# Performance work log

Measured on AMD Instinct MI355X. Metric: run time of the kernel, lower is better.

Reference implementation:

```python
import jax, jax.numpy as jnp
import numpy as np

EMBED_DIM = 512
NUM_HEADS = 8
B, L_Q, L_K = 2, 2048, 2048


def setup_inputs() -> dict:
    key = jax.random.key(0)
    ks = jax.random.split(key, 8)
    s = 0.02  # weight init scale
    return {
        "query": jax.random.normal(ks[0], (B, L_Q, EMBED_DIM), jnp.float32),
        "key":   jax.random.normal(ks[1], (B, L_K, EMBED_DIM), jnp.float32),
        "value": jax.random.normal(ks[2], (B, L_K, EMBED_DIM), jnp.float32),
        "wq": jax.random.normal(ks[3], (EMBED_DIM, EMBED_DIM), jnp.float32) * s,
        "wk": jax.random.normal(ks[4], (EMBED_DIM, EMBED_DIM), jnp.float32) * s,
        "wv": jax.random.normal(ks[5], (EMBED_DIM, EMBED_DIM), jnp.float32) * s,
        "bq": jnp.zeros((EMBED_DIM,), jnp.float32),
        "bk": jnp.zeros((EMBED_DIM,), jnp.float32),
        "bv": jnp.zeros((EMBED_DIM,), jnp.float32),
        "wo": jax.random.normal(ks[6], (EMBED_DIM, EMBED_DIM), jnp.float32) * s,
        "bo": jnp.zeros((EMBED_DIM,), jnp.float32),
    }


def _prob_sparse_mask(query, key, num_heads):
    # Faithful to _prob_QK: max-mean sparsity score, top-k query selection,
    # gather of reduced queries, reduced QK matmul (vectorized, no python loops).
    Bq, Lq, D = query.shape
    Lk = key.shape[1]
    dh = D // num_heads
    n_top = int(np.log(Lk))  # int(np.ceil/np.log) as in source forward: int(np.log(L_K))
    Q = query.reshape(Bq, Lq, num_heads, dh)
    K = key.reshape(Bq, Lk, num_heads, dh)
    Qh = jnp.transpose(Q, (0, 2, 1, 3))                      # [B,H,Lq,dh]
    # NOTE: source does K.transpose(1,2).reshape(B,H,D,L_K) -- a reshape, not a
    # transpose of the last two dims. We replicate that exactly.
    Kr = jnp.transpose(K, (0, 2, 1, 3)).reshape(Bq, num_heads, dh, Lk)  # [B,H,dh,Lk]
    QK = jnp.einsum('bhqd,bhdk->bhqk', Qh, Kr)               # [B,H,Lq,Lk]
    M = QK.max(-1) - QK.sum(-1) / Lk                         # max-mean score [B,H,Lq]
    _, M_top = jax.lax.top_k(M, n_top)                       # [B,H,n_top]
    Q_red = jnp.take_along_axis(Qh, M_top[..., None], axis=2)  # [B,H,n_top,dh]
    QK_red = jnp.einsum('bhtd,bhdk->bhtk', Q_red, Kr)        # [B,H,n_top,Lk]
    # Scatter reduced rows back into a full additive attn mask (zeros elsewhere).
    mask = jnp.zeros((Bq, num_heads, Lq, Lk), QK.dtype)
    bi = jnp.arange(Bq)[:, None, None]
    hi = jnp.arange(num_heads)[None, :, None]
    return mask.at[bi, hi, M_top].set(QK_red)


def reference(query, key, value, wq, wk, wv, bq, bk, bv, wo, bo):
    Bq, Lq, D = query.shape
    Lk = key.shape[1]
    H = NUM_HEADS
    dh = D // H
    mask = _prob_sparse_mask(query, key, H)                  # [B,H,Lq,Lk]
    q = (query @ wq.T + bq).reshape(Bq, Lq, H, dh).transpose(0, 2, 1, 3)
    k = (key @ wk.T + bk).reshape(Bq, Lk, H, dh).transpose(0, 2, 1, 3)
    v = (value @ wv.T + bv).reshape(Bq, Lk, H, dh).transpose(0, 2, 1, 3)
    scores = jnp.einsum('bhqd,bhkd->bhqk', q, k) * (dh ** -0.5) + mask
    attn = jax.nn.softmax(scores, axis=-1)                   # dropout inactive (eval)
    out = jnp.einsum('bhqk,bhkd->bhqd', attn, v)
    out = out.transpose(0, 2, 1, 3).reshape(Bq, Lq, D)
    return out @ wo.T + bo
```

## Files before the change

kernel.cpp:

```cpp
#include <hip/hip_runtime.h>
#include <type_traits>

#define DEV static __device__ __forceinline__

typedef short s16;
typedef __attribute__((ext_vector_type(4))) short short4_t;
typedef __attribute__((ext_vector_type(8))) short short8;
typedef __attribute__((ext_vector_type(4))) float f32x4;
typedef __attribute__((ext_vector_type(16))) float f32x16;

#define NB 2
#define NH 8
#define SL 2048
#define DM 512
#define DH 64
#define NTOP 7
#define LOG2E 1.4426950408889634f
#define NROWS (NB*NH*SL)
#define FSPLIT 4
#define SSPLIT 4

DEV short f2bf(float x){
  union { float f; unsigned u; } v; v.f = x;
  unsigned r = v.u + 0x7fffu + ((v.u >> 16) & 1u);
  return (short)(r >> 16);
}
DEV float bf2f(short b){
  union { float f; unsigned u; } v; v.u = ((unsigned)(unsigned short)b) << 16;
  return v.f;
}
DEV f32x4 mfma16(short8 a, short8 b, f32x4 c){
  return __builtin_amdgcn_mfma_f32_16x16x32_bf16(a, b, c, 0, 0, 0);
}
DEV f32x16 mfma32(short8 a, short8 b, f32x16 c){
  return __builtin_amdgcn_mfma_f32_32x32x16_bf16(a, b, c, 0, 0, 0);
}
DEV unsigned cvtpk(float lo, float hi){
  unsigned r;
  asm("v_cvt_pk_bf16_f32 %0, %1, %2" : "=v"(r) : "v"(lo), "v"(hi));
  return r;
}
DEV void gl2lds16(const s16* g, s16* l){
  __builtin_amdgcn_global_load_lds(
      (const __attribute__((address_space(1))) unsigned*)g,
      (__attribute__((address_space(3))) unsigned*)l, 16, 0, 0);
}

__global__ void prep_kernel(const float* __restrict__ query, const float* __restrict__ key,
    const float* __restrict__ value,
    const float* __restrict__ wq, const float* __restrict__ wk,
    const float* __restrict__ wv, const float* __restrict__ wo,
    s16* __restrict__ q_hi, s16* __restrict__ q_lo, s16* __restrict__ xk, s16* __restrict__ xv,
    s16* __restrict__ khi, s16* __restrict__ klo,
    s16* __restrict__ wqb, s16* __restrict__ wkb, s16* __restrict__ wvb, s16* __restrict__ wob){
  const int nbb = (NB*SL*DM)/256;
  const int wbb = (DM*DM)/256;
  __shared__ s16 thi[64][66];
  __shared__ s16 tlo[64][66];
  int bid = blockIdx.x;
  int t = threadIdx.x;
  if (bid < nbb){
    int i = bid*256 + t;
    float v = query[i];
    short h = f2bf(v);
    q_hi[i] = h;
    q_lo[i] = f2bf(v - bf2f(h));
    return;
  }
  bid -= nbb;
  if (bid < nbb){ int i = bid*256 + t; xk[i] = f2bf(key[i]); return; }
  bid -= nbb;
  if (bid < nbb){ int i = bid*256 + t; xv[i] = f2bf(value[i]); return; }
  bid -= nbb;
  if (bid < 512){
    int k6 = bid & 31, h = (bid >> 5) & 7, b = bid >> 8;
    int kl = t & 63, dq = t >> 6;
    #pragma unroll
    for (int dd = 0; dd < 16; ++dd){
      int d = dd*4 + dq;
      float v = key[((size_t)b*SL + d*32 + k6)*DM + h*DH + kl];
      short hh = f2bf(v);
      thi[d][kl] = hh;
      tlo[d][kl] = f2bf(v - bf2f(hh));
    }
    __syncthreads();
    int d2 = t & 63, kq = t >> 6;
    size_t obase = (((size_t)(b*NH + h))*SL + (size_t)k6*64)*DH;
    #pragma unroll
    for (int kk = 0; kk < 16; ++kk){
      int kl2 = kk*4 + kq;
      khi[obase + (size_t)kl2*DH + d2] = thi[d2][kl2];
      klo[obase + (size_t)kl2*DH + d2] = tlo[d2][kl2];
    }
    return;
  }
  bid -= 512;
  if (bid < wbb){ int i = bid*256 + t; wqb[i] = f2bf(wq[i]); return; }
  bid -= wbb;
  if (bid < wbb){ int i = bid*256 + t; wkb[i] = f2bf(wk[i]); return; }
  bid -= wbb;
  if (bid < wbb){ int i = bid*256 + t; wvb[i] = f2bf(wv[i]); return; }
  bid -= wbb;
  if (bid < wbb){ int i = bid*256 + t; wob[i] = f2bf(wo[i]); return; }
}

__global__ __launch_bounds__(256) void vpt_kernel(const s16* __restrict__ Vp, s16* __restrict__ VpT){
  __shared__ s16 tl[64][66];
  int bid = blockIdx.x;
  int k6 = bid & 31, h = (bid >> 5) & 7, b = bid >> 8;
  int t = threadIdx.x;
  int d = t & 63, kq = t >> 6;
  #pragma unroll
  for (int kk = 0; kk < 16; ++kk){
    int kl = kk*4 + kq;
    tl[kl][d] = Vp[((size_t)b*SL + k6*64 + kl)*DM + h*DH + d];
  }
  __syncthreads();
  int kl2 = t & 63, dq = t >> 6;
  size_t obase = ((size_t)(b*NH + h))*DH*SL + (size_t)k6*64;
  #pragma unroll
  for (int dd = 0; dd < 16; ++dd){
    int d2 = dd*4 + dq;
    VpT[obase + (size_t)d2*SL + kl2] = tl[kl2][d2];
  }
}

template<int OUTF32>
DEV void gemm_body(const s16* __restrict__ A, const s16* __restrict__ Bw,
        const float* __restrict__ bias, void* __restrict__ Cout, int bid, int tid, float scale){
  __shared__ __align__(16) s16 Abuf[2][128*64];
  __shared__ __align__(16) s16 Bbuf[2][64*64];
  int nt = bid >> 3, ot = bid & 7;
  int w = tid >> 6, l = tid & 63;
  int lr = l & 15, lg = l >> 4;
  int n0 = nt*128, o0 = ot*64;
  auto stage = [&](int cur, int kg){
    #pragma unroll
    for (int i = 0; i < 4; ++i){
      int r = w*32 + i*8 + (l>>3);
      int cs = (l&7) ^ (r&7);
      gl2lds16(A + (size_t)(n0 + r)*DM + kg + cs*8, &Abuf[cur][(w*32 + i*8)*64]);
    }
    #pragma unroll
    for (int i = 0; i < 2; ++i){
      int r = w*16 + i*8 + (l>>3);
      int cs = (l&7) ^ (r&7);
      gl2lds16(Bw + (size_t)(o0 + r)*DM + kg + cs*8, &Bbuf[cur][(w*16 + i*8)*64]);
    }
  };
  f32x4 acc[2][4] = {};
  stage(0, 0);
  __syncthreads();
  const int NIT = DM/64;
  for (int it = 0; it < NIT; ++it){
    int cur = it & 1;
    if (it + 1 < NIT) stage(cur^1, (it+1)*64);
    #pragma unroll
    for (int kc = 0; kc < 2; ++kc){
      short8 a0 = *(const short8*)&Abuf[cur][(w*32 +      lr)*64 + ((kc*4+lg) ^ (lr&7))*8];
      short8 a1 = *(const short8*)&Abuf[cur][(w*32 + 16 + lr)*64 + ((kc*4+lg) ^ (lr&7))*8];
      #pragma unroll
      for (int c = 0; c < 4; ++c){
        short8 bf = *(const short8*)&Bbuf[cur][(c*16 + lr)*64 + ((kc*4+lg) ^ (lr&7))*8];
        acc[0][c] = mfma16(a0, bf, acc[0][c]);
        acc[1][c] = mfma16(a1, bf, acc[1][c]);
      }
    }
    __syncthreads();
  }
  #pragma unroll
  for (int sub = 0; sub < 2; ++sub)
    #pragma unroll
    for (int c = 0; c < 4; ++c){
      int col = o0 + c*16 + lr;
      float bb = bias[col];
      #pragma unroll
      for (int j = 0; j < 4; ++j){
        int row = n0 + w*32 + sub*16 + lg*4 + j;
        float v = (acc[sub][c][j] + bb)*scale;
        if (OUTF32) ((float*)Cout)[(size_t)row*DM + col] = v;
        else        ((s16*) Cout)[(size_t)row*DM + col] = f2bf(v);
      }
    }
}

__global__ __launch_bounds__(256) void gemm_proj(const s16* __restrict__ Aq, const s16* __restrict__ Ak,
        const s16* __restrict__ Av, const s16* __restrict__ Wq, const s16* __restrict__ Wk,
        const s16* __restrict__ Wv, const float* __restrict__ bq, const float* __restrict__ bk,
        const float* __restrict__ bv, s16* __restrict__ Oq, s16* __restrict__ Ok, s16* __restrict__ Ov){
  int which = blockIdx.x >> 8;
  const s16* A  = which == 0 ? Aq : which == 1 ? Ak : Av;
  const s16* Bw = which == 0 ? Wq : which == 1 ? Wk : Wv;
  const float* bias = which == 0 ? bq : which == 1 ? bk : bv;
  s16* C = which == 0 ? Oq : which == 1 ? Ok : Ov;
  float scale = which == 0 ? 0.125f*LOG2E : 1.0f;
  gemm_body<0>(A, Bw, bias, C, blockIdx.x & 255, threadIdx.x, scale);
}

__global__ __launch_bounds__(256) void gemm_out(const s16* __restrict__ A, const s16* __restrict__ Bw,
        const float* __restrict__ bias, float* __restrict__ Cout){
  gemm_body<1>(A, Bw, bias, Cout, blockIdx.x, threadIdx.x, 1.0f);
}

__global__ __launch_bounds__(512) void stats_kernel(const s16* __restrict__ qhi, const s16* __restrict__ qlo,
        const s16* __restrict__ khi, const s16* __restrict__ klo,
        float* __restrict__ Mmx, float* __restrict__ Msm){
  __shared__ __align__(16) s16 Hbuf[2][64*64];
  __shared__ __align__(16) s16 Lbuf[2][64*64];
  int bid = blockIdx.x;
  int s = bid & 3, qt = (bid >> 2) & 15, h = (bid >> 6) & 7, b = bid >> 9;
  int tid = threadIdx.x;
  int w = tid >> 6, l = tid & 63;
  int lr = l & 15, lg = l >> 4;
  int dx = lr & 7;
  int q0 = qt*128 + w*16;
  const s16* qp  = qhi + ((size_t)b*SL + q0 + lr)*DM + h*DH + lg*8;
  const s16* qlp = qlo + ((size_t)b*SL + q0 + lr)*DM + h*DH + lg*8;
  short8 qh0 = *(const short8*)qp;
  short8 qh1 = *(const short8*)(qp + 32);
  short8 ql0 = *(const short8*)qlp;
  short8 ql1 = *(const short8*)(qlp + 32);
  const s16* kb  = khi + ((size_t)b*NH + h)*SL*DH;
  const s16* klb = klo + ((size_t)b*NH + h)*SL*DH;
  const s16* hR0 = &Hbuf[0][lr*64 + ((lg      ^ dx)*8)];
  const s16* hR1 = &Hbuf[0][lr*64 + (((4+lg) ^ dx)*8)];
  const s16* lR0 = &Lbuf[0][lr*64 + ((lg      ^ dx)*8)];
  const s16* lR1 = &Lbuf[0][lr*64 + (((4+lg) ^ dx)*8)];
  int rS = tid >> 3;
  int slot = tid & 7;
  int cs = slot ^ (rS & 7);
  int kbeg = s*(SL/SSPLIT);
  const int NT = (SL/SSPLIT)/64;
  f32x4 hreg, lreg;
  auto loadr = [&](int t){
    int kg = kbeg + t*64;
    hreg = *(const f32x4*)(kb  + (size_t)(kg + rS)*DH + cs*8);
    lreg = *(const f32x4*)(klb + (size_t)(kg + rS)*DH + cs*8);
  };
  auto writer = [&](int buf){
    *(f32x4*)&Hbuf[buf][rS*64 + slot*8] = hreg;
    *(f32x4*)&Lbuf[buf][rS*64 + slot*8] = lreg;
  };
  float mx = -1e30f, sm = 0.f;
  auto body = [&](auto CURC){
    constexpr int CUR = decltype(CURC)::value;
    #pragma unroll
    for (int t = 0; t < 4; ++t){
      short8 kh0 = *(const short8*)(hR0 + CUR*4096 + t*1024);
      short8 kh1 = *(const short8*)(hR1 + CUR*4096 + t*1024);
      short8 kl0 = *(const short8*)(lR0 + CUR*4096 + t*1024);
      short8 kl1 = *(const short8*)(lR1 + CUR*4096 + t*1024);
      f32x4 sacc = {};
      sacc = mfma16(kh0, qh0, sacc);
      sacc = mfma16(kh1, qh1, sacc);
      sacc = mfma16(kl0, qh0, sacc);
      sacc = mfma16(kl1, qh1, sacc);
      sacc = mfma16(kh0, ql0, sacc);
      sacc = mfma16(kh1, ql1, sacc);
      #pragma unroll
      for (int j = 0; j < 4; ++j){ mx = fmaxf(mx, sacc[j]); sm += sacc[j]; }
    }
  };
  loadr(0);
  writer(0);
  loadr(1);
  __syncthreads();
  auto step = [&](auto TC){
    constexpr int T = decltype(TC)::value;
    if constexpr (T + 1 < NT) writer((T+1)&1);
    if constexpr (T + 2 < NT) loadr(T+2);
    body(std::integral_constant<int, T&1>{});
    __syncthreads();
  };
  step(std::integral_constant<int,0>{}); step(std::integral_constant<int,1>{});
  step(std::integral_constant<int,2>{}); step(std::integral_constant<int,3>{});
  step(std::integral_constant<int,4>{}); step(std::integral_constant<int,5>{});
  step(std::integral_constant<int,6>{}); step(std::integral_constant<int,7>{});
  mx = fmaxf(mx, __shfl_xor(mx, 16));
  mx = fmaxf(mx, __shfl_xor(mx, 32));
  sm += __shfl_xor(sm, 16);
  sm += __shfl_xor(sm, 32);
  if (lg == 0){
    size_t row = ((size_t)b*NH + h)*SL + q0 + lr;
    Mmx[(size_t)s*NROWS + row] = mx;
    Msm[(size_t)s*NROWS + row] = sm;
  }
}

__global__ __launch_bounds__(256) void topk_kernel(const float* __restrict__ Mmx,
        const float* __restrict__ Msm, int* __restrict__ topidx, int* __restrict__ rowsel){
  int bh = blockIdx.x;
  int t = threadIdx.x;
  int w = t >> 6, l = t & 63;
  __shared__ float smv[SL];
  __shared__ float rv[4];
  __shared__ int   ri[4];
  size_t base = (size_t)bh*SL;
  for (int i = t; i < SL; i += 256){
    float mx = Mmx[base + i];
    float sm = Msm[base + i];
    #pragma unroll
    for (int s = 1; s < SSPLIT; ++s){
      mx = fmaxf(mx, Mmx[(size_t)s*NROWS + base + i]);
      sm += Msm[(size_t)s*NROWS + base + i];
    }
    smv[i] = mx - sm*(1.0f/SL);
    rowsel[base + i] = -1;
  }
  __syncthreads();
  for (int tt = 0; tt < NTOP; ++tt){
    float bvv = -1e38f; int bi = SL;
    for (int i = t; i < SL; i += 256){
      float v = smv[i];
      if (v > bvv){ bvv = v; bi = i; }
    }
    #pragma unroll
    for (int off = 32; off >= 1; off >>= 1){
      float ov = __shfl_xor(bvv, off);
      int oi = __shfl_xor(bi, off);
      if (ov > bvv || (ov == bvv && oi < bi)){ bvv = ov; bi = oi; }
    }
    if (l == 0){ rv[w] = bvv; ri[w] = bi; }
    __syncthreads();
    if (t == 0){
      float bv2 = rv[0]; int bi2 = ri[0];
      #pragma unroll
      for (int ww = 1; ww < 4; ++ww)
        if (rv[ww] > bv2 || (rv[ww] == bv2 && ri[ww] < bi2)){ bv2 = rv[ww]; bi2 = ri[ww]; }
      topidx[bh*8 + tt] = bi2;
      rowsel[base + bi2] = tt;
      smv[bi2] = -1e38f;
    }
    __syncthreads();
  }
}

__global__ __launch_bounds__(256) void maskrow_kernel(const float* __restrict__ query,
        const float* __restrict__ key, const int* __restrict__ topidx, float* __restrict__ maskrows){
  __shared__ float tile[64][65];
  __shared__ float qs[NTOP][64];
  int bid = blockIdx.x;
  int k6 = bid & 31, h = (bid >> 5) & 7, b = bid >> 8;
  int bh = b*NH + h;
  int t = threadIdx.x;
  int kl = t & 63, w = t >> 6;
  for (int i = t; i < NTOP*64; i += 256){
    int tt = i >> 6, d = i & 63;
    qs[tt][d] = query[((size_t)b*SL + topidx[bh*8 + tt])*DM + h*DH + d];
  }
  #pragma unroll
  for (int dd = 0; dd < 16; ++dd){
    int d = dd*4 + w;
    tile[d][kl] = key[((size_t)b*SL + d*32 + k6)*DM + h*DH + kl];
  }
  __syncthreads();
  for (int tt = w; tt < NTOP; tt += 4){
    float acc = 0.f;
    #pragma unroll
    for (int d = 0; d < 64; ++d)
      acc = fmaf(qs[tt][d], tile[d][kl], acc);
    maskrows[((size_t)bh*NTOP + tt)*SL + k6*64 + kl] = acc*LOG2E;
  }
}

__global__ __launch_bounds__(256, 3) void flash_kernel(const s16* __restrict__ Qp,
        const s16* __restrict__ Kp, const s16* __restrict__ VpT,
        const float* __restrict__ maskrows, const int* __restrict__ rowsel,
        float* __restrict__ Opart, float* __restrict__ lpart){
  __shared__ __align__(16) s16 SB[4*64*64];
  int bid = blockIdx.x;
  int s = bid & 3, qt = (bid >> 2) & 15, h = (bid >> 6) & 7, b = bid >> 9;
  int tid = threadIdx.x;
  int w = tid >> 6, l = tid & 63;
  int ln = l & 31, lh = l >> 5;
  int q0 = qt*128 + w*32;
  int bh = b*NH + h;
  const s16* qp = Qp + ((size_t)b*SL + q0 + ln)*DM + h*DH + lh*8;
  short8 bq[4];
  #pragma unroll
  for (int kc = 0; kc < 4; ++kc) bq[kc] = *(const short8*)(qp + kc*16);
  int sel = rowsel[(size_t)bh*SL + q0 + ln];
  const float* mrow = maskrows + ((size_t)bh*NTOP + (sel >= 0 ? sel : 0))*SL;
  const s16* kpb = Kp + (size_t)b*SL*DM + h*DH;
  const s16* vtb = VpT + (size_t)bh*DH*SL;
  const s16* kR[2][4];
  #pragma unroll
  for (int g = 0; g < 2; ++g)
    #pragma unroll
    for (int kc = 0; kc < 4; ++kc)
      kR[g][kc] = &SB[(g*32 + ln)*64 + (((kc*2 + lh) ^ (ln & 7))*8)];
  int r8 = l >> 3;
  int slot = l & 7;
  int cs = slot ^ (r8 & 7);
  int kbeg = s*(SL/FSPLIT);
  const int NT = (SL/FSPLIT)/64;
  f32x4 kreg[2], vreg[2];
  auto loadr = [&](int t){
    int kg = kbeg + t*64;
    #pragma unroll
    for (int c = 0; c < 2; ++c){
      int r = c*32 + w*8 + r8;
      kreg[c] = *(const f32x4*)(kpb + (size_t)(kg + r)*DM + cs*8);
      vreg[c] = *(const f32x4*)(vtb + (size_t)r*SL + kg + cs*8);
    }
  };
  auto writer = [&](int buf){
    #pragma unroll
    for (int c = 0; c < 2; ++c){
      int r = c*32 + w*8 + r8;
      *(f32x4*)&SB[(size_t)buf*4096 + r*64 + slot*8] = kreg[c];
      *(f32x4*)&SB[8192 + (size_t)buf*4096 + r*64 + slot*8] = vreg[c];
    }
  };
  short8 ones;
  #pragma unroll
  for (int i = 0; i < 8; ++i) ones[i] = (short)0x3F80;
  f32x16 accO[2] = {};
  f32x16 accL = {};
  auto body = [&](auto CURC, int k0){
    constexpr int CB = decltype(CURC)::value * 8192;
    f32x16 S[2] = {};
    __builtin_amdgcn_s_setprio(1);
    #pragma unroll
    for (int g = 0; g < 2; ++g)
      #pragma unroll
      for (int kc = 0; kc < 4; ++kc){
        short8 kf = *(const short8*)((const char*)kR[g][kc] + CB);
        S[g] = mfma32(kf, bq[kc], S[g]);
      }
    __builtin_amdgcn_s_setprio(0);
    if (sel >= 0){
      #pragma unroll
      for (int g = 0; g < 2; ++g)
        #pragma unroll
        for (int rq = 0; rq < 4; ++rq)
          #pragma unroll
          for (int j = 0; j < 4; ++j)
            S[g][rq*4 + j] += mrow[k0 + g*32 + rq*8 + lh*4 + j];
    }
    #pragma unroll
    for (int g = 0; g < 2; ++g)
      #pragma unroll
      for (int e = 0; e < 16; ++e)
        S[g][e] = exp2f(S[g][e]);
    unsigned W[2][8];
    #pragma unroll
    for (int g = 0; g < 2; ++g)
      #pragma unroll
      for (int t = 0; t < 8; ++t)
        W[g][t] = cvtpk(S[g][2*t], S[g][2*t+1]);
    short8 pf[4];
    #pragma unroll
    for (int kc = 0; kc < 4; ++kc){
      int g = kc >> 1, j = kc & 1;
      unsigned a0 = W[g][4*j + 0], a1 = W[g][4*j + 2];
      asm("v_permlane32_swap_b32 %0, %1" : "+v"(a0), "+v"(a1));
      unsigned b0 = W[g][4*j + 1], b1 = W[g][4*j + 3];
      asm("v_permlane32_swap_b32 %0, %1" : "+v"(b0), "+v"(b1));
      union { unsigned u[4]; short8 s8; } uu;
      uu.u[0] = a0; uu.u[1] = b0; uu.u[2] = a1; uu.u[3] = b1;
      pf[kc] = uu.s8;
    }
    __builtin_amdgcn_s_setprio(1);
    #pragma unroll
    for (int kc = 0; kc < 4; ++kc)
      accL = mfma32(ones, pf[kc], accL);
    #pragma unroll
    for (int dg = 0; dg < 2; ++dg)
      #pragma unroll
      for (int kc = 0; kc < 4; ++kc){
        short8 vf = *(const short8*)((const char*)kR[dg][kc] + CB + 16384);
        accO[dg] = mfma32(vf, pf[kc], accO[dg]);
      }
    __builtin_amdgcn_s_setprio(0);
  };
  loadr(0);
  writer(0);
  loadr(1);
  __syncthreads();
  auto step = [&](auto TC){
    constexpr int T = decltype(TC)::value;
    if constexpr (T + 1 < NT) writer((T+1)&1);
    if constexpr (T + 2 < NT) loadr(T+2);
    body(std::integral_constant<int, T&1>{}, kbeg + T*64);
    __syncthreads();
  };
  step(std::integral_constant<int,0>{}); step(std::integral_constant<int,1>{});
  step(std::integral_constant<int,2>{}); step(std::integral_constant<int,3>{});
  step(std::integral_constant<int,4>{}); step(std::integral_constant<int,5>{});
  step(std::integral_constant<int,6>{}); step(std::integral_constant<int,7>{});
  size_t row = (size_t)bh*SL + q0 + ln;
  float* Op = Opart + ((size_t)s*NROWS + row)*DH;
  #pragma unroll
  for (int dg = 0; dg < 2; ++dg)
    #pragma unroll
    for (int rq = 0; rq < 4; ++rq){
      f32x4 v = { accO[dg][rq*4+0], accO[dg][rq*4+1], accO[dg][rq*4+2], accO[dg][rq*4+3] };
      *(f32x4*)(Op + dg*32 + rq*8 + lh*4) = v;
    }
  if (lh == 0)
    lpart[(size_t)s*NROWS + row] = accL[0];
}

__global__ __launch_bounds__(256) void flash_combine(const float* __restrict__ Opart,
        const float* __restrict__ lpart, s16* __restrict__ outh){
  int row = blockIdx.x*4 + (threadIdx.x >> 6);
  int d = threadIdx.x & 63;
  float L = 0.f, o = 0.f;
  #pragma unroll
  for (int s = 0; s < FSPLIT; ++s){
    L += lpart[(size_t)s*NROWS + row];
    o += Opart[((size_t)s*NROWS + row)*DH + d];
  }
  o /= L;
  int b = row >> 14, h = (row >> 11) & 7, q = row & (SL - 1);
  outh[((size_t)b*SL + q)*DM + h*DH + d] = f2bf(o);
}

extern "C" void kernel_launch(void* const* d_in, const int* in_sizes, int n_in,
                              void* d_out, int out_size, void* d_ws, size_t ws_size,
                              hipStream_t stream){
  (void)in_sizes; (void)n_in; (void)out_size;
  const float* query = (const float*)d_in[0];
  const float* key   = (const float*)d_in[1];
  const float* value = (const float*)d_in[2];
  const float* wq    = (const float*)d_in[3];
  const float* wk    = (const float*)d_in[4];
  const float* wv    = (const float*)d_in[5];
  const float* bq    = (const float*)d_in[6];
  const float* bk    = (const float*)d_in[7];
  const float* bv    = (const float*)d_in[8];
  const float* wo    = (const float*)d_in[9];
  const float* bo    = (const float*)d_in[10];

  const size_t NE = (size_t)NB*SL*DM;
  const size_t WE = (size_t)DM*DM;

  char* p = (char*)d_ws;
  size_t off = 0;
  auto alloc = [&](size_t n)->char*{ char* r = p + off; off += (n + 255) & ~(size_t)255; return r; };
  s16* wob = (s16*)alloc(WE*2);
  s16* Qp  = (s16*)alloc(NE*2);
  s16* Kp  = (s16*)alloc(NE*2);
  s16* VpT = (s16*)alloc(NE*2);
  float* maskrows = (float*)alloc((size_t)NB*NH*NTOP*SL*4);
  int* topidx   = (int*)alloc((size_t)NB*NH*8*4);
  int* rowsel   = (int*)alloc((size_t)NROWS*4);
  float* Mmx    = (float*)alloc((size_t)SSPLIT*NROWS*4);
  float* Msm    = (float*)alloc((size_t)SSPLIT*NROWS*4);
  float* lpart  = (float*)alloc((size_t)FSPLIT*NROWS*4);
  float* Opart  = (float*)alloc((size_t)FSPLIT*NROWS*DH*4);
  s16* outh = (s16*)alloc(NE*2);
  s16* q_hi = (s16*)alloc(NE*2);
  s16* q_lo = (s16*)alloc(NE*2);
  s16* xk   = (s16*)alloc(NE*2);
  s16* xv   = (s16*)alloc(NE*2);
  s16* khatT_hi = (s16*)alloc(NE*2);
  s16* khatT_lo = (s16*)alloc(NE*2);
  s16* wqb = (s16*)alloc(WE*2);
  s16* wkb = (s16*)alloc(WE*2);
  s16* wvb = (s16*)alloc(WE*2);
  s16* Vp  = (s16*)alloc(NE*2);
  if (off > ws_size) return;

  const int nbb = (int)(NE/256);
  const int wbb = (int)(WE/256);
  prep_kernel<<<3*nbb + 512 + 4*wbb, 256, 0, stream>>>(query, key, value, wq, wk, wv, wo,
      q_hi, q_lo, xk, xv, khatT_hi, khatT_lo, wqb, wkb, wvb, wob);

  gemm_proj<<<3*256, 256, 0, stream>>>(q_hi, xk, xv, wqb, wkb, wvb, bq, bk, bv, Qp, Kp, Vp);
  vpt_kernel<<<512, 256, 0, stream>>>(Vp, VpT);

  stats_kernel<<<NB*NH*(SL/128)*SSPLIT, 512, 0, stream>>>(q_hi, q_lo, khatT_hi, khatT_lo, Mmx, Msm);
  topk_kernel<<<NB*NH, 256, 0, stream>>>(Mmx, Msm, topidx, rowsel);
  maskrow_kernel<<<512, 256, 0, stream>>>(query, key, topidx, maskrows);

  flash_kernel<<<NB*NH*(SL/128)*FSPLIT, 256, 0, stream>>>(Qp, Kp, VpT, maskrows, rowsel,
      Opart, lpart);
  flash_combine<<<NROWS/4, 256, 0, stream>>>(Opart, lpart, outh);
  gemm_out<<<256, 256, 0, stream>>>(outh, wob, bo, (float*)d_out);
}
```

Measured before the change: 143.5 us.

## Use single-bf16 stats screening with exact fp32 rescoring of top candidates

```diff
diff --git a/kernel.cpp b/kernel.cpp
--- a/kernel.cpp
+++ b/kernel.cpp
@@ -4,7 +4,6 @@
 #define DEV static __device__ __forceinline__
 
 typedef short s16;
-typedef __attribute__((ext_vector_type(4))) short short4_t;
 typedef __attribute__((ext_vector_type(8))) short short8;
 typedef __attribute__((ext_vector_type(4))) float f32x4;
 typedef __attribute__((ext_vector_type(16))) float f32x16;
@@ -15,6 +14,7 @@
 #define DM 512
 #define DH 64
 #define NTOP 7
+#define NCAND 16
 #define LOG2E 1.4426950408889634f
 #define NROWS (NB*NH*SL)
 #define FSPLIT 4
@@ -25,10 +25,6 @@
   unsigned r = v.u + 0x7fffu + ((v.u >> 16) & 1u);
   return (short)(r >> 16);
 }
-DEV float bf2f(short b){
-  union { float f; unsigned u; } v; v.u = ((unsigned)(unsigned short)b) << 16;
-  return v.f;
-}
 DEV f32x4 mfma16(short8 a, short8 b, f32x4 c){
   return __builtin_amdgcn_mfma_f32_16x16x32_bf16(a, b, c, 0, 0, 0);
 }
@@ -50,23 +46,15 @@
     const float* __restrict__ value,
     const float* __restrict__ wq, const float* __restrict__ wk,
     const float* __restrict__ wv, const float* __restrict__ wo,
-    s16* __restrict__ q_hi, s16* __restrict__ q_lo, s16* __restrict__ xk, s16* __restrict__ xv,
-    s16* __restrict__ khi, s16* __restrict__ klo,
+    s16* __restrict__ xq, s16* __restrict__ xk, s16* __restrict__ xv,
+    s16* __restrict__ khat,
     s16* __restrict__ wqb, s16* __restrict__ wkb, s16* __restrict__ wvb, s16* __restrict__ wob){
   const int nbb = (NB*SL*DM)/256;
   const int wbb = (DM*DM)/256;
   __shared__ s16 thi[64][66];
-  __shared__ s16 tlo[64][66];
   int bid = blockIdx.x;
   int t = threadIdx.x;
-  if (bid < nbb){
-    int i = bid*256 + t;
-    float v = query[i];
-    short h = f2bf(v);
-    q_hi[i] = h;
-    q_lo[i] = f2bf(v - bf2f(h));
-    return;
-  }
+  if (bid < nbb){ int i = bid*256 + t; xq[i] = f2bf(query[i]); return; }
   bid -= nbb;
   if (bid < nbb){ int i = bid*256 + t; xk[i] = f2bf(key[i]); return; }
   bid -= nbb;
@@ -78,10 +66,7 @@
     #pragma unroll
     for (int dd = 0; dd < 16; ++dd){
       int d = dd*4 + dq;
-      float v = key[((size_t)b*SL + d*32 + k6)*DM + h*DH + kl];
-      short hh = f2bf(v);
-      thi[d][kl] = hh;
-      tlo[d][kl] = f2bf(v - bf2f(hh));
+      thi[d][kl] = f2bf(key[((size_t)b*SL + d*32 + k6)*DM + h*DH + kl]);
     }
     __syncthreads();
     int d2 = t & 63, kq = t >> 6;
@@ -89,8 +74,7 @@
     #pragma unroll
     for (int kk = 0; kk < 16; ++kk){
       int kl2 = kk*4 + kq;
-      khi[obase + (size_t)kl2*DH + d2] = thi[d2][kl2];
-      klo[obase + (size_t)kl2*DH + d2] = tlo[d2][kl2];
+      khat[obase + (size_t)kl2*DH + d2] = thi[d2][kl2];
     }
     return;
   }
@@ -202,11 +186,9 @@
   gemm_body<1>(A, Bw, bias, Cout, blockIdx.x, threadIdx.x, 1.0f);
 }
 
-__global__ __launch_bounds__(512) void stats_kernel(const s16* __restrict__ qhi, const s16* __restrict__ qlo,
-        const s16* __restrict__ khi, const s16* __restrict__ klo,
-        float* __restrict__ Mmx, float* __restrict__ Msm){
+__global__ __launch_bounds__(512) void stats_kernel(const s16* __restrict__ xq,
+        const s16* __restrict__ khat, float* __restrict__ Mmx, float* __restrict__ Msm){
   __shared__ __align__(16) s16 Hbuf[2][64*64];
-  __shared__ __align__(16) s16 Lbuf[2][64*64];
   int bid = blockIdx.x;
   int s = bid & 3, qt = (bid >> 2) & 15, h = (bid >> 6) & 7, b = bid >> 9;
   int tid = threadIdx.x;
@@ -214,32 +196,23 @@
   int lr = l & 15, lg = l >> 4;
   int dx = lr & 7;
   int q0 = qt*128 + w*16;
-  const s16* qp  = qhi + ((size_t)b*SL + q0 + lr)*DM + h*DH + lg*8;
-  const s16* qlp = qlo + ((size_t)b*SL + q0 + lr)*DM + h*DH + lg*8;
+  const s16* qp = xq + ((size_t)b*SL + q0 + lr)*DM + h*DH + lg*8;
   short8 qh0 = *(const short8*)qp;
   short8 qh1 = *(const short8*)(qp + 32);
-  short8 ql0 = *(const short8*)qlp;
-  short8 ql1 = *(const short8*)(qlp + 32);
-  const s16* kb  = khi + ((size_t)b*NH + h)*SL*DH;
-  const s16* klb = klo + ((size_t)b*NH + h)*SL*DH;
+  const s16* kb = khat + ((size_t)b*NH + h)*SL*DH;
   const s16* hR0 = &Hbuf[0][lr*64 + ((lg      ^ dx)*8)];
   const s16* hR1 = &Hbuf[0][lr*64 + (((4+lg) ^ dx)*8)];
-  const s16* lR0 = &Lbuf[0][lr*64 + ((lg      ^ dx)*8)];
-  const s16* lR1 = &Lbuf[0][lr*64 + (((4+lg) ^ dx)*8)];
   int rS = tid >> 3;
   int slot = tid & 7;
   int cs = slot ^ (rS & 7);
   int kbeg = s*(SL/SSPLIT);
   const int NT = (SL/SSPLIT)/64;
-  f32x4 hreg, lreg;
+  f32x4 hreg;
   auto loadr = [&](int t){
-    int kg = kbeg + t*64;
-    hreg = *(const f32x4*)(kb  + (size_t)(kg + rS)*DH + cs*8);
-    lreg = *(const f32x4*)(klb + (size_t)(kg + rS)*DH + cs*8);
+    hreg = *(const f32x4*)(kb + (size_t)(kbeg + t*64 + rS)*DH + cs*8);
   };
   auto writer = [&](int buf){
     *(f32x4*)&Hbuf[buf][rS*64 + slot*8] = hreg;
-    *(f32x4*)&Lbuf[buf][rS*64 + slot*8] = lreg;
   };
   float mx = -1e30f, sm = 0.f;
   auto body = [&](auto CURC){
@@ -248,15 +221,9 @@
     for (int t = 0; t < 4; ++t){
       short8 kh0 = *(const short8*)(hR0 + CUR*4096 + t*1024);
       short8 kh1 = *(const short8*)(hR1 + CUR*4096 + t*1024);
-      short8 kl0 = *(const short8*)(lR0 + CUR*4096 + t*1024);
-      short8 kl1 = *(const short8*)(lR1 + CUR*4096 + t*1024);
       f32x4 sacc = {};
       sacc = mfma16(kh0, qh0, sacc);
       sacc = mfma16(kh1, qh1, sacc);
-      sacc = mfma16(kl0, qh0, sacc);
-      sacc = mfma16(kl1, qh1, sacc);
-      sacc = mfma16(kh0, ql0, sacc);
-      sacc = mfma16(kh1, ql1, sacc);
       #pragma unroll
       for (int j = 0; j < 4; ++j){ mx = fmaxf(mx, sacc[j]); sm += sacc[j]; }
     }
@@ -288,7 +255,7 @@
 }
 
 __global__ __launch_bounds__(256) void topk_kernel(const float* __restrict__ Mmx,
-        const float* __restrict__ Msm, int* __restrict__ topidx, int* __restrict__ rowsel){
+        const float* __restrict__ Msm, int* __restrict__ candidx, int* __restrict__ rowsel){
   int bh = blockIdx.x;
   int t = threadIdx.x;
   int w = t >> 6, l = t & 63;
@@ -308,7 +275,7 @@
     rowsel[base + i] = -1;
   }
   __syncthreads();
-  for (int tt = 0; tt < NTOP; ++tt){
+  for (int tt = 0; tt < NCAND; ++tt){
     float bvv = -1e38f; int bi = SL;
     for (int i = t; i < SL; i += 256){
       float v = smv[i];
@@ -327,26 +294,26 @@
       #pragma unroll
       for (int ww = 1; ww < 4; ++ww)
         if (rv[ww] > bv2 || (rv[ww] == bv2 && ri[ww] < bi2)){ bv2 = rv[ww]; bi2 = ri[ww]; }
-      topidx[bh*8 + tt] = bi2;
-      rowsel[base + bi2] = tt;
+      candidx[bh*NCAND + tt] = bi2;
       smv[bi2] = -1e38f;
     }
     __syncthreads();
   }
 }
 
-__global__ __launch_bounds__(256) void maskrow_kernel(const float* __restrict__ query,
-        const float* __restrict__ key, const int* __restrict__ topidx, float* __restrict__ maskrows){
+__global__ __launch_bounds__(256) void cand_kernel(const float* __restrict__ query,
+        const float* __restrict__ key, const int* __restrict__ candidx,
+        float* __restrict__ candrows, float* __restrict__ cmx, float* __restrict__ csm){
   __shared__ float tile[64][65];
-  __shared__ float qs[NTOP][64];
+  __shared__ float qs[NCAND][64];
   int bid = blockIdx.x;
   int k6 = bid & 31, h = (bid >> 5) & 7, b = bid >> 8;
   int bh = b*NH + h;
   int t = threadIdx.x;
   int kl = t & 63, w = t >> 6;
-  for (int i = t; i < NTOP*64; i += 256){
+  for (int i = t; i < NCAND*64; i += 256){
     int tt = i >> 6, d = i & 63;
-    qs[tt][d] = query[((size_t)b*SL + topidx[bh*8 + tt])*DM + h*DH + d];
+    qs[tt][d] = query[((size_t)b*SL + candidx[bh*NCAND + tt])*DM + h*DH + d];
   }
   #pragma unroll
   for (int dd = 0; dd < 16; ++dd){
@@ -354,18 +321,59 @@
     tile[d][kl] = key[((size_t)b*SL + d*32 + k6)*DM + h*DH + kl];
   }
   __syncthreads();
-  for (int tt = w; tt < NTOP; tt += 4){
+  for (int tt = w; tt < NCAND; tt += 4){
     float acc = 0.f;
     #pragma unroll
     for (int d = 0; d < 64; ++d)
       acc = fmaf(qs[tt][d], tile[d][kl], acc);
-    maskrows[((size_t)bh*NTOP + tt)*SL + k6*64 + kl] = acc*LOG2E;
+    candrows[((size_t)bh*NCAND + tt)*SL + k6*64 + kl] = acc*LOG2E;
+    float mx = acc, sm = acc;
+    #pragma unroll
+    for (int off = 1; off < 64; off <<= 1){
+      mx = fmaxf(mx, __shfl_xor(mx, off));
+      sm += __shfl_xor(sm, off);
+    }
+    if (kl == 0){
+      cmx[((size_t)bh*NCAND + tt)*32 + k6] = mx;
+      csm[((size_t)bh*NCAND + tt)*32 + k6] = sm;
+    }
+  }
+}
+
+__global__ __launch_bounds__(64) void topsel_kernel(const float* __restrict__ cmx,
+        const float* __restrict__ csm, const int* __restrict__ candidx, int* __restrict__ rowsel){
+  int bh = blockIdx.x;
+  int l = threadIdx.x;
+  __shared__ float Mex[NCAND];
+  if (l < NCAND){
+    float mx = -1e38f, sm = 0.f;
+    #pragma unroll 4
+    for (int p = 0; p < 32; ++p){
+      mx = fmaxf(mx, cmx[((size_t)bh*NCAND + l)*32 + p]);
+      sm += csm[((size_t)bh*NCAND + l)*32 + p];
+    }
+    Mex[l] = mx - sm*(1.0f/SL);
+  }
+  __syncthreads();
+  if (l == 0){
+    unsigned used = 0;
+    for (int tt = 0; tt < NTOP; ++tt){
+      float bv = -1e38f; int bslot = 0; int brow = 1 << 30;
+      for (int c = 0; c < NCAND; ++c){
+        if (used & (1u << c)) continue;
+        int row = candidx[bh*NCAND + c];
+        float v = Mex[c];
+        if (v > bv || (v == bv && row < brow)){ bv = v; bslot = c; brow = row; }
+      }
+      used |= 1u << bslot;
+      rowsel[(size_t)bh*SL + brow] = bslot;
+    }
   }
 }
 
 __global__ __launch_bounds__(256, 3) void flash_kernel(const s16* __restrict__ Qp,
         const s16* __restrict__ Kp, const s16* __restrict__ VpT,
-        const float* __restrict__ maskrows, const int* __restrict__ rowsel,
+        const float* __restrict__ candrows, const int* __restrict__ rowsel,
         float* __restrict__ Opart, float* __restrict__ lpart){
   __shared__ __align__(16) s16 SB[4*64*64];
   int bid = blockIdx.x;
@@ -380,7 +388,7 @@
   #pragma unroll
   for (int kc = 0; kc < 4; ++kc) bq[kc] = *(const short8*)(qp + kc*16);
   int sel = rowsel[(size_t)bh*SL + q0 + ln];
-  const float* mrow = maskrows + ((size_t)bh*NTOP + (sel >= 0 ? sel : 0))*SL;
+  const float* mrow = candrows + ((size_t)bh*NCAND + (sel >= 0 ? sel : 0))*SL;
   const s16* kpb = Kp + (size_t)b*SL*DM + h*DH;
   const s16* vtb = VpT + (size_t)bh*DH*SL;
   const s16* kR[2][4];
@@ -388,10 +396,10 @@
   for (int g = 0; g < 2; ++g)
     #pragma unroll
     for (int kc = 0; kc < 4; ++kc)
-      kR[g][kc] = &SB[(g*32 + ln)*64 + (((kc*2 + lh) ^ (ln & 7))*8)];
+      kR[g][kc] = &SB[(g*32 + ln)*64 + ((((kc*2 + lh) ^ (ln & 7) ^ ((ln >> 3) & 3))*8))];
   int r8 = l >> 3;
   int slot = l & 7;
-  int cs = slot ^ (r8 & 7);
+  int cs = slot ^ r8 ^ w;
   int kbeg = s*(SL/FSPLIT);
   const int NT = (SL/FSPLIT)/64;
   f32x4 kreg[2], vreg[2];
@@ -543,20 +551,20 @@
   s16* Qp  = (s16*)alloc(NE*2);
   s16* Kp  = (s16*)alloc(NE*2);
   s16* VpT = (s16*)alloc(NE*2);
-  float* maskrows = (float*)alloc((size_t)NB*NH*NTOP*SL*4);
-  int* topidx   = (int*)alloc((size_t)NB*NH*8*4);
+  float* candrows = (float*)alloc((size_t)NB*NH*NCAND*SL*4);
+  int* candidx  = (int*)alloc((size_t)NB*NH*NCAND*4);
+  float* cmx    = (float*)alloc((size_t)NB*NH*NCAND*32*4);
+  float* csm    = (float*)alloc((size_t)NB*NH*NCAND*32*4);
   int* rowsel   = (int*)alloc((size_t)NROWS*4);
   float* Mmx    = (float*)alloc((size_t)SSPLIT*NROWS*4);
   float* Msm    = (float*)alloc((size_t)SSPLIT*NROWS*4);
   float* lpart  = (float*)alloc((size_t)FSPLIT*NROWS*4);
   float* Opart  = (float*)alloc((size_t)FSPLIT*NROWS*DH*4);
   s16* outh = (s16*)alloc(NE*2);
-  s16* q_hi = (s16*)alloc(NE*2);
-  s16* q_lo = (s16*)alloc(NE*2);
+  s16* xq   = (s16*)alloc(NE*2);
   s16* xk   = (s16*)alloc(NE*2);
   s16* xv   = (s16*)alloc(NE*2);
-  s16* khatT_hi = (s16*)alloc(NE*2);
-  s16* khatT_lo = (s16*)alloc(NE*2);
+  s16* khat = (s16*)alloc(NE*2);
   s16* wqb = (s16*)alloc(WE*2);
   s16* wkb = (s16*)alloc(WE*2);
   s16* wvb = (s16*)alloc(WE*2);
@@ -566,16 +574,17 @@
   const int nbb = (int)(NE/256);
   const int wbb = (int)(WE/256);
   prep_kernel<<<3*nbb + 512 + 4*wbb, 256, 0, stream>>>(query, key, value, wq, wk, wv, wo,
-      q_hi, q_lo, xk, xv, khatT_hi, khatT_lo, wqb, wkb, wvb, wob);
-
-  gemm_proj<<<3*256, 256, 0, stream>>>(q_hi, xk, xv, wqb, wkb, wvb, bq, bk, bv, Qp, Kp, Vp);
+      xq, xk, xv, khat, wqb, wkb, wvb, wob);
+
+  gemm_proj<<<3*256, 256, 0, stream>>>(xq, xk, xv, wqb, wkb, wvb, bq, bk, bv, Qp, Kp, Vp);
   vpt_kernel<<<512, 256, 0, stream>>>(Vp, VpT);
 
-  stats_kernel<<<NB*NH*(SL/128)*SSPLIT, 512, 0, stream>>>(q_hi, q_lo, khatT_hi, khatT_lo, Mmx, Msm);
-  topk_kernel<<<NB*NH, 256, 0, stream>>>(Mmx, Msm, topidx, rowsel);
-  maskrow_kernel<<<512, 256, 0, stream>>>(query, key, topidx, maskrows);
-
-  flash_kernel<<<NB*NH*(SL/128)*FSPLIT, 256, 0, stream>>>(Qp, Kp, VpT, maskrows, rowsel,
+  stats_kernel<<<NB*NH*(SL/128)*SSPLIT, 512, 0, stream>>>(xq, khat, Mmx, Msm);
+  topk_kernel<<<NB*NH, 256, 0, stream>>>(Mmx, Msm, candidx, rowsel);
+  cand_kernel<<<512, 256, 0, stream>>>(query, key, candidx, candrows, cmx, csm);
+  topsel_kernel<<<NB*NH, 64, 0, stream>>>(cmx, csm, candidx, rowsel);
+
+  flash_kernel<<<NB*NH*(SL/128)*FSPLIT, 256, 0, stream>>>(Qp, Kp, VpT, candrows, rowsel,
       Opart, lpart);
   flash_combine<<<NROWS/4, 256, 0, stream>>>(Opart, lpart, outh);
   gemm_out<<<256, 256, 0, stream>>>(outh, wob, bo, (float*)d_out);
```

New measurement: 149.2 us. +4.0%, slower.
